# Optimization experiments

Measured on AMD Instinct MI355X. Metric: run time of the kernel, lower is better.

The kernel has to match this reference:

```python
import jax, jax.numpy as jnp
import numpy as np

B, T, F, D, H, L = 4, 1024, 128, 512, 8, 4
DFF = 4 * D
NE, MD = 16, 20
HD = D // H
SCALE = 1.0 / HD ** 0.5


def _ln(x, w, b):
    m = jnp.mean(x, axis=-1, keepdims=True)
    v = jnp.mean((x - m) ** 2, axis=-1, keepdims=True)
    return (x - m) * jax.lax.rsqrt(v + 1e-5) * w + b


def setup_inputs() -> dict:
    key = jax.random.key(0)
    ks = jax.random.split(key, 16)
    rn = lambda k, shape: jax.random.normal(k, shape, jnp.float32) * 0.02
    return {
        'node_features': jax.random.normal(ks[0], (B, T, F), jnp.float32),
        'centrality': jax.random.uniform(ks[1], (B, T), jnp.float32),
        'edge_types': jax.random.randint(ks[2], (B, T, T), 0, NE),
        'sp_dist': jax.random.randint(ks[3], (B, T, T), 0, MD + 1),
        'node_W': rn(ks[4], (F, D)), 'node_b': jnp.zeros((D,), jnp.float32),
        'cent_W': rn(ks[5], (D,)), 'cent_b': jnp.zeros((D,), jnp.float32),
        'edge_emb': rn(ks[6], (NE, H)), 'dist_emb': rn(ks[7], (MD + 1, H)),
        'ln1_w': jnp.ones((L, D), jnp.float32), 'ln1_b': jnp.zeros((L, D), jnp.float32),
        'q_W': rn(ks[8], (L, D, D)), 'q_b': jnp.zeros((L, D), jnp.float32),
        'k_W': rn(ks[9], (L, D, D)), 'k_b': jnp.zeros((L, D), jnp.float32),
        'v_W': rn(ks[10], (L, D, D)), 'v_b': jnp.zeros((L, D), jnp.float32),
        'o_W': rn(ks[11], (L, D, D)), 'o_b': jnp.zeros((L, D), jnp.float32),
        'ln2_w': jnp.ones((L, D), jnp.float32), 'ln2_b': jnp.zeros((L, D), jnp.float32),
        'f1_W': rn(ks[12], (L, D, DFF)), 'f1_b': jnp.zeros((L, DFF), jnp.float32),
        'f2_W': rn(ks[13], (L, DFF, D)), 'f2_b': jnp.zeros((L, D), jnp.float32),
    }


def _forward(node_features, centrality, edge_types, sp_dist,
             node_W, node_b, cent_W, cent_b, edge_emb, dist_emb,
             ln1_w, ln1_b, q_W, q_b, k_W, k_b, v_W, v_b, o_W, o_b,
             ln2_w, ln2_b, f1_W, f1_b, f2_W, f2_b):
    # node embedding + centrality encoding
    h = node_features @ node_W + node_b                      # [B,T,D]
    h = h + centrality[..., None] * cent_W + cent_b          # Linear(1,D)
    # Graphormer attention bias: [B,T,T,H] -> [B,H,T,T]
    sp = jnp.clip(sp_dist, 0, MD)
    attn_bias = (edge_emb[edge_types] + dist_emb[sp]).transpose(0, 3, 1, 2)

    def step(h, p):
        l1w, l1b, qW, qb, kW, kb, vW, vb, oW, ob, l2w, l2b, w1, b1, w2, b2 = p
        x = _ln(h, l1w, l1b)
        q = (x @ qW + qb).reshape(B, T, H, HD)
        k = (x @ kW + kb).reshape(B, T, H, HD)
        v = (x @ vW + vb).reshape(B, T, H, HD)
        scores = jnp.einsum('bihd,bjhd->bhij', q, k) * SCALE + attn_bias
        attn = jax.nn.softmax(scores, axis=-1)
        o = jnp.einsum('bhij,bjhd->bihd', attn, v).reshape(B, T, D)
        h = h + (o @ oW + ob)                                # dropout in eval mode
        x2 = _ln(h, l2w, l2b)
        h = h + (jax.nn.silu(x2 @ w1 + b1) @ w2 + b2)
        return h, None

    layer_params = (ln1_w, ln1_b, q_W, q_b, k_W, k_b, v_W, v_b, o_W, o_b,
                    ln2_w, ln2_b, f1_W, f1_b, f2_W, f2_b)
    h, _ = jax.lax.scan(step, h, layer_params)
    return h


def reference(node_features, centrality, edge_types, sp_dist,
              node_W, node_b, cent_W, cent_b, edge_emb, dist_emb,
              ln1_w, ln1_b, q_W, q_b, k_W, k_b, v_W, v_b, o_W, o_b,
              ln2_w, ln2_b, f1_W, f1_b, f2_W, f2_b):
    return _forward(node_features, centrality, edge_types, sp_dist,
                    node_W, node_b, cent_W, cent_b, edge_emb, dist_emb,
                    ln1_w, ln1_b, q_W, q_b, k_W, k_b, v_W, v_b, o_W, o_b,
                    ln2_w, ln2_b, f1_W, f1_b, f2_W, f2_b)
```

## Files before the change

kernel.cpp:

```cpp
#include <hip/hip_runtime.h>
#include <cstddef>
#include <cstdint>

#define B_    4
#define T_    1024
#define F_    128
#define D_    512
#define H_    8
#define L_    4
#define DFF_  2048
#define HD_   64
#define SCALE_ 0.125f
#define LOG2E_ 1.4426950408889634f
#define CL2E_  (SCALE_ * LOG2E_)

typedef __attribute__((ext_vector_type(8))) short bf16x8;
typedef __attribute__((ext_vector_type(4))) float f32x4;

#define AS1(p) ((const __attribute__((address_space(1))) void*)(p))
#define AS3(p) ((__attribute__((address_space(3))) void*)(p))

__device__ __forceinline__ short f2bf(float f) {
    unsigned u = __float_as_uint(f);
    u += 0x7FFFu + ((u >> 16) & 1u);
    return (short)(u >> 16);
}
__device__ __forceinline__ float bf2f(short s) {
    return __uint_as_float(((unsigned)(unsigned short)s) << 16);
}

__global__ __launch_bounds__(256) void ln_k(
    const float* __restrict__ X, const float* __restrict__ w,
    const float* __restrict__ b, short* __restrict__ Y)
{
    const int row = blockIdx.x;
    const int tid = threadIdx.x;
    const float* xr = X + (size_t)row * D_;
    const float v0 = xr[tid];
    const float v1 = xr[tid + 256];
    float s  = v0 + v1;
    float s2 = v0 * v0 + v1 * v1;
#pragma unroll
    for (int off = 1; off < 64; off <<= 1) {
        s  += __shfl_xor(s,  off);
        s2 += __shfl_xor(s2, off);
    }
    __shared__ float ss[4], ss2[4];
    if ((tid & 63) == 0) { ss[tid >> 6] = s; ss2[tid >> 6] = s2; }
    __syncthreads();
    s  = ss[0]  + ss[1]  + ss[2]  + ss[3];
    s2 = ss2[0] + ss2[1] + ss2[2] + ss2[3];
    const float mean = s * (1.f / D_);
    const float var  = s2 * (1.f / D_) - mean * mean;
    const float r    = rsqrtf(var + 1e-5f);
    short* yr = Y + (size_t)row * D_;
    yr[tid]       = f2bf((v0 - mean) * r * w[tid]       + b[tid]);
    yr[tid + 256] = f2bf((v1 - mean) * r * w[tid + 256] + b[tid + 256]);
}

__global__ __launch_bounds__(256) void transpose_all_k(
    const float* __restrict__ qW, const float* __restrict__ kW,
    const float* __restrict__ vW, const float* __restrict__ oW,
    const float* __restrict__ f1W, const float* __restrict__ f2W,
    const float* __restrict__ nW,
    short* __restrict__ WqkvT, short* __restrict__ WoT,
    short* __restrict__ Wf1T, short* __restrict__ Wf2T,
    short* __restrict__ nWt)
{
    const int id = blockIdx.y;
    const float* src; short* dst; int K, N;
    if (id < 12) {
        const int l = id / 3, which = id % 3;
        const float* s3 = (which == 0) ? qW : (which == 1) ? kW : vW;
        src = s3 + (size_t)l * D_ * D_;
        dst = WqkvT + ((size_t)l * 3 + which) * D_ * D_;
        K = D_; N = D_;
    } else if (id < 16) {
        const int l = id - 12;
        src = oW + (size_t)l * D_ * D_;  dst = WoT + (size_t)l * D_ * D_;
        K = D_; N = D_;
    } else if (id < 20) {
        const int l = id - 16;
        src = f1W + (size_t)l * D_ * DFF_;  dst = Wf1T + (size_t)l * DFF_ * D_;
        K = D_; N = DFF_;
    } else if (id < 24) {
        const int l = id - 20;
        src = f2W + (size_t)l * DFF_ * D_;  dst = Wf2T + (size_t)l * D_ * DFF_;
        K = DFF_; N = D_;
    } else {
        src = nW; dst = nWt; K = F_; N = D_;
    }
    const int ntiles = (K >> 5) * (N >> 5);
    if ((int)blockIdx.x >= ntiles) return;
    const int nt = N >> 5;
    const int k0 = (blockIdx.x / nt) << 5, n0 = (blockIdx.x % nt) << 5;

    __shared__ float t[32][33];
    const int c = threadIdx.x, r0 = threadIdx.y;
#pragma unroll
    for (int i = 0; i < 32; i += 8)
        t[r0 + i][c] = src[(size_t)(k0 + r0 + i) * N + n0 + c];
    __syncthreads();
#pragma unroll
    for (int i = 0; i < 32; i += 8)
        dst[(size_t)(n0 + r0 + i) * K + k0 + c] = f2bf(t[c][r0 + i]);
}

__global__ __launch_bounds__(256) void prep_k(
    const int* __restrict__ et, const int* __restrict__ sp,
    const float* __restrict__ ee, const float* __restrict__ de,
    unsigned char* __restrict__ biasT8,
    const float* __restrict__ nf, short* __restrict__ nfb,
    const float* __restrict__ qb, const float* __restrict__ kb,
    const float* __restrict__ vb, float* __restrict__ biasf)
{
    const int bid = blockIdx.x;
    const int tid = threadIdx.x;
    if (bid >= 4096) {
        if (bid < 4608) {
            const int i = (((bid - 4096) << 8) + tid) << 2;
            const float4 v = *(const float4*)(nf + i);
            *(short4*)(nfb + i) =
                make_short4(f2bf(v.x), f2bf(v.y), f2bf(v.z), f2bf(v.w));
        } else {
            const int i = ((bid - 4608) << 8) + tid;
            const int l = i / 1536, c = i % 1536;
            float v;
            if (c < 512)       v = qb[l * 512 + c];
            else if (c < 1024) v = kb[l * 512 + c - 512];
            else               v = vb[l * 512 + c - 1024];
            biasf[i] = v;
        }
        return;
    }
    __shared__ float eeS[16][8], deS[21][8];
    if (tid < 128) eeS[tid >> 3][tid & 7] = ee[tid];
    for (int t = tid; t < 168; t += 256)
        deS[t >> 3][t & 7] = de[t];
    __syncthreads();
    const int gid = bid * 256 + tid;
    const int j4  = (gid & 255) << 2;
    const int bi  = gid >> 8;
    const size_t base = (size_t)bi * T_ + j4;
    const int4 e = *(const int4*)(et + base);
    const int4 s = *(const int4*)(sp + base);
    const int b = bi >> 10, i = bi & 1023;
    const int ex[4] = {e.x, e.y, e.z, e.w};
    const int sx[4] = {min(s.x, 20), min(s.y, 20), min(s.z, 20), min(s.w, 20)};
#pragma unroll
    for (int h = 0; h < 8; ++h) {
        uchar4 o;
        float v;
        v = (eeS[ex[0]][h] + deS[sx[0]][h]) * LOG2E_ + 0.5f;
        o.x = (unsigned char)(int)fminf(fmaxf(v * 255.f + 0.5f, 0.f), 255.f);
        v = (eeS[ex[1]][h] + deS[sx[1]][h]) * LOG2E_ + 0.5f;
        o.y = (unsigned char)(int)fminf(fmaxf(v * 255.f + 0.5f, 0.f), 255.f);
        v = (eeS[ex[2]][h] + deS[sx[2]][h]) * LOG2E_ + 0.5f;
        o.z = (unsigned char)(int)fminf(fmaxf(v * 255.f + 0.5f, 0.f), 255.f);
        v = (eeS[ex[3]][h] + deS[sx[3]][h]) * LOG2E_ + 0.5f;
        o.w = (unsigned char)(int)fminf(fmaxf(v * 255.f + 0.5f, 0.f), 255.f);
        *(uchar4*)(biasT8 + ((size_t)((b * H_ + h) * T_ + i)) * T_ + j4) = o;
    }
}

__global__ __launch_bounds__(256) void embed_mm_k(
    const short* __restrict__ A, const short* __restrict__ Wt,
    const float* __restrict__ nb, const float* __restrict__ cb,
    const float* __restrict__ cW, const float* __restrict__ cent,
    float* __restrict__ C)
{
    const int K = F_, N = D_;
    __shared__ short As[128 * 32];
    __shared__ short Bs[64 * 32];
    const int tid  = threadIdx.x;
    const int lane = tid & 63, wv = tid >> 6;
    const int bm = blockIdx.y << 7, bn = blockIdx.x << 6;
    const int wm = (wv & 1) << 6, wn = (wv >> 1) << 5;

    const int c0 = (wv << 6) + lane;
    const int m0 = c0 >> 2, q0 = (c0 & 3) ^ ((m0 >> 1) & 3);
    const int c1 = 256 + c0;
    const int m1 = c1 >> 2, q1 = (c1 & 3) ^ ((m1 >> 1) & 3);

    const short* gA0 = A  + (size_t)(bm + m0) * K + (q0 << 3);
    const short* gA1 = A  + (size_t)(bm + m1) * K + (q1 << 3);
    const short* gB0 = Wt + (size_t)(bn + m0) * K + (q0 << 3);

    f32x4 acc[4][2];
#pragma unroll
    for (int i = 0; i < 4; ++i)
#pragma unroll
        for (int j = 0; j < 2; ++j)
            acc[i][j] = (f32x4){0.f, 0.f, 0.f, 0.f};

    const int fm = lane & 15, fq = lane >> 4;
    int caddr[4], baddr[2];
#pragma unroll
    for (int t = 0; t < 4; ++t) {
        const int rowA = wm + (t << 4) + fm;
        caddr[t] = ((rowA << 2) + (fq ^ ((rowA >> 1) & 3))) << 3;
    }
#pragma unroll
    for (int t = 0; t < 2; ++t) {
        const int rowB = wn + (t << 4) + fm;
        baddr[t] = ((rowB << 2) + (fq ^ ((rowB >> 1) & 3))) << 3;
    }

    for (int k0 = 0; k0 < K; k0 += 32) {
        __builtin_amdgcn_global_load_lds(AS1(gA0), AS3(As + (wv << 9)),        16, 0, 0);
        __builtin_amdgcn_global_load_lds(AS1(gA1), AS3(As + 2048 + (wv << 9)), 16, 0, 0);
        __builtin_amdgcn_global_load_lds(AS1(gB0), AS3(Bs + (wv << 9)),        16, 0, 0);
        gA0 += 32; gA1 += 32; gB0 += 32;
        __syncthreads();

        bf16x8 af[4], bf[2];
#pragma unroll
        for (int t = 0; t < 4; ++t) af[t] = *(const bf16x8*)(As + caddr[t]);
#pragma unroll
        for (int t = 0; t < 2; ++t) bf[t] = *(const bf16x8*)(Bs + baddr[t]);
#pragma unroll
        for (int i = 0; i < 4; ++i)
#pragma unroll
            for (int j = 0; j < 2; ++j)
                acc[i][j] = __builtin_amdgcn_mfma_f32_16x16x32_bf16(
                    af[i], bf[j], acc[i][j], 0, 0, 0);
        __syncthreads();
    }

    const int col0 = bn + wn + fm;
    const int row0 = bm + wm + (fq << 2);
#pragma unroll
    for (int j = 0; j < 2; ++j) {
        const int colg = col0 + (j << 4);
        const float bb = nb[colg] + cb[colg];
        const float cw = cW[colg];
#pragma unroll
        for (int i = 0; i < 4; ++i) {
#pragma unroll
            for (int r = 0; r < 4; ++r) {
                const int rowg = row0 + (i << 4) + r;
                C[(size_t)rowg * N + colg] = acc[i][j][r] + bb + cent[rowg] * cw;
            }
        }
    }
}

template <int OUTM, int ACT, int RES>
__global__ __launch_bounds__(256) void mm_k(
    const short* __restrict__ A, const short* __restrict__ Wt,
    const float* __restrict__ bias, const float* __restrict__ R,
    void* __restrict__ Cv, int M, int N, int K)
{
    __shared__ short As[128 * 32];
    __shared__ short Bs[128 * 32];
    const int tid  = threadIdx.x;
    const int lane = tid & 63, wv = tid >> 6;
    const int bm = blockIdx.y << 7, bn = blockIdx.x << 7;
    const int wm = (wv & 1) << 6, wn = (wv >> 1) << 6;

    const int c0 = (wv << 6) + lane;
    const int m0 = c0 >> 2, q0 = (c0 & 3) ^ ((m0 >> 1) & 3);
    const int c1 = 256 + c0;
    const int m1 = c1 >> 2, q1 = (c1 & 3) ^ ((m1 >> 1) & 3);

    const short* gA0 = A  + (size_t)(bm + m0) * K + (q0 << 3);
    const short* gA1 = A  + (size_t)(bm + m1) * K + (q1 << 3);
    const short* gB0 = Wt + (size_t)(bn + m0) * K + (q0 << 3);
    const short* gB1 = Wt + (size_t)(bn + m1) * K + (q1 << 3);

    f32x4 acc[4][4];
#pragma unroll
    for (int i = 0; i < 4; ++i)
#pragma unroll
        for (int j = 0; j < 4; ++j)
            acc[i][j] = (f32x4){0.f, 0.f, 0.f, 0.f};

    const int fm = lane & 15, fq = lane >> 4;
    int caddr[4], baddr[4];
#pragma unroll
    for (int t = 0; t < 4; ++t) {
        const int rowA = wm + (t << 4) + fm;
        caddr[t] = ((rowA << 2) + (fq ^ ((rowA >> 1) & 3))) << 3;
        const int rowB = wn + (t << 4) + fm;
        baddr[t] = ((rowB << 2) + (fq ^ ((rowB >> 1) & 3))) << 3;
    }

    for (int k0 = 0; k0 < K; k0 += 32) {
        __builtin_amdgcn_global_load_lds(AS1(gA0), AS3(As + (wv << 9)),        16, 0, 0);
        __builtin_amdgcn_global_load_lds(AS1(gA1), AS3(As + 2048 + (wv << 9)), 16, 0, 0);
        __builtin_amdgcn_global_load_lds(AS1(gB0), AS3(Bs + (wv << 9)),        16, 0, 0);
        __builtin_amdgcn_global_load_lds(AS1(gB1), AS3(Bs + 2048 + (wv << 9)), 16, 0, 0);
        gA0 += 32; gA1 += 32; gB0 += 32; gB1 += 32;
        __syncthreads();

        bf16x8 af[4], bf[4];
#pragma unroll
        for (int t = 0; t < 4; ++t) {
            af[t] = *(const bf16x8*)(As + caddr[t]);
            bf[t] = *(const bf16x8*)(Bs + baddr[t]);
        }
#pragma unroll
        for (int i = 0; i < 4; ++i)
#pragma unroll
            for (int j = 0; j < 4; ++j)
                acc[i][j] = __builtin_amdgcn_mfma_f32_16x16x32_bf16(
                    af[i], bf[j], acc[i][j], 0, 0, 0);
        __syncthreads();
    }

    const int col0 = bn + wn + fm;
    const int row0 = bm + wm + (fq << 2);
    float* Cf = (float*)Cv;
    short* Cb = (short*)Cv;
#pragma unroll
    for (int j = 0; j < 4; ++j) {
        const int colg = col0 + (j << 4);
        const float bb = bias[colg];
#pragma unroll
        for (int i = 0; i < 4; ++i) {
#pragma unroll
            for (int r = 0; r < 4; ++r) {
                const int rowg = row0 + (i << 4) + r;
                float v = acc[i][j][r] + bb;
                if (ACT) v = v / (1.f + __expf(-v));
                const size_t off = (size_t)rowg * N + colg;
                if (RES) v += R[off];
                if (OUTM == 1) Cb[off] = f2bf(v);
                else           Cf[off] = v;
            }
        }
    }
}

__global__ __launch_bounds__(256) void qkv64_k(
    const short* __restrict__ A, const short* __restrict__ Wt,
    const float* __restrict__ bias, short* __restrict__ QKb,
    short* __restrict__ VtOut)
{
    const int K = D_;
    __shared__ short As[128 * 32];
    __shared__ short Bs[64 * 32];
    const int tid  = threadIdx.x;
    const int lane = tid & 63, wv = tid >> 6;
    const int bm = blockIdx.y << 7, bn = blockIdx.x << 6;
    const int wm = (wv & 1) << 6, wn = (wv >> 1) << 5;

    const int c0 = (wv << 6) + lane;
    const int m0 = c0 >> 2, q0 = (c0 & 3) ^ ((m0 >> 1) & 3);
    const int c1 = 256 + c0;
    const int m1 = c1 >> 2, q1 = (c1 & 3) ^ ((m1 >> 1) & 3);

    const short* gA0 = A  + (size_t)(bm + m0) * K + (q0 << 3);
    const short* gA1 = A  + (size_t)(bm + m1) * K + (q1 << 3);
    const short* gB0 = Wt + (size_t)(bn + m0) * K + (q0 << 3);

    f32x4 acc[4][2];
#pragma unroll
    for (int i = 0; i < 4; ++i)
#pragma unroll
        for (int j = 0; j < 2; ++j)
            acc[i][j] = (f32x4){0.f, 0.f, 0.f, 0.f};

    const int fm = lane & 15, fq = lane >> 4;
    int caddr[4], baddr[2];
#pragma unroll
    for (int t = 0; t < 4; ++t) {
        const int rowA = wm + (t << 4) + fm;
        caddr[t] = ((rowA << 2) + (fq ^ ((rowA >> 1) & 3))) << 3;
    }
#pragma unroll
    for (int t = 0; t < 2; ++t) {
        const int rowB = wn + (t << 4) + fm;
        baddr[t] = ((rowB << 2) + (fq ^ ((rowB >> 1) & 3))) << 3;
    }

    for (int k0 = 0; k0 < K; k0 += 32) {
        __builtin_amdgcn_global_load_lds(AS1(gA0), AS3(As + (wv << 9)),        16, 0, 0);
        __builtin_amdgcn_global_load_lds(AS1(gA1), AS3(As + 2048 + (wv << 9)), 16, 0, 0);
        __builtin_amdgcn_global_load_lds(AS1(gB0), AS3(Bs + (wv << 9)),        16, 0, 0);
        gA0 += 32; gA1 += 32; gB0 += 32;
        __syncthreads();

        bf16x8 af[4], bf[2];
#pragma unroll
        for (int t = 0; t < 4; ++t) af[t] = *(const bf16x8*)(As + caddr[t]);
#pragma unroll
        for (int t = 0; t < 2; ++t) bf[t] = *(const bf16x8*)(Bs + baddr[t]);
#pragma unroll
        for (int i = 0; i < 4; ++i)
#pragma unroll
            for (int j = 0; j < 2; ++j)
                acc[i][j] = __builtin_amdgcn_mfma_f32_16x16x32_bf16(
                    af[i], bf[j], acc[i][j], 0, 0, 0);
        __syncthreads();
    }

    const int col0 = bn + wn + fm;
    const int row0 = bm + wm + (fq << 2);
#pragma unroll
    for (int j = 0; j < 2; ++j) {
        const int colg = col0 + (j << 4);
        const float bb = bias[colg];
#pragma unroll
        for (int i = 0; i < 4; ++i) {
#pragma unroll
            for (int r = 0; r < 4; ++r) {
                const int rowg = row0 + (i << 4) + r;
                const float v = acc[i][j][r] + bb;
                if (colg < 1024) {
                    QKb[(size_t)rowg * 1024 + colg] = f2bf(v);
                } else {
                    const int da = colg - 1024;
                    const int hh = da >> 6, dd = da & 63;
                    const int bb2 = rowg >> 10, tt = rowg & 1023;
                    VtOut[((size_t)(bb2 * H_ + hh) * 64 + dd) * T_ + tt] = f2bf(v);
                }
            }
        }
    }
}

__global__ __launch_bounds__(256) void flash_k(
    const short* __restrict__ QKb, const short* __restrict__ Vt,
    const unsigned char* __restrict__ biasT8, short* __restrict__ OpartB,
    float* __restrict__ Lpart)
{
    const int tid = threadIdx.x;
    const int bx = blockIdx.x;
    const int it = bx >> 1, split = bx & 1;
    const int i0 = it << 6;
    const int h  = blockIdx.y;
    const int b  = blockIdx.z;
    const int lane = tid & 63, w = tid >> 6;
    const int fm = lane & 15, q = lane >> 4;

    __shared__ short Ks[4096];
    __shared__ short Vs[4096];
    __shared__ unsigned char Bsh8[4096];
    __shared__ short Ps[64][72];

    const short* qp = QKb + (size_t)(b * T_ + i0 + (w << 4) + fm) * 1024 + (h << 6) + (q << 3);
    const bf16x8 aq0 = *(const bf16x8*)(qp);
    const bf16x8 aq1 = *(const bf16x8*)(qp + 32);

    const int s0 = (w << 6) + lane, r0 = s0 >> 3, cc0 = (s0 & 7) ^ (r0 & 7);
    const int s1 = 256 + s0,        r1 = s1 >> 3, cc1 = (s1 & 7) ^ (r1 & 7);
    const short* gK0 = QKb + (size_t)(b * T_ + r0) * 1024 + 512 + (h << 6) + (cc0 << 3);
    const short* gK1 = QKb + (size_t)(b * T_ + r1) * 1024 + 512 + (h << 6) + (cc1 << 3);
    const short* gV0 = Vt + ((size_t)((b * H_ + h) << 6) + r0) * T_ + (cc0 << 3);
    const short* gV1 = Vt + ((size_t)((b * H_ + h) << 6) + r1) * T_ + (cc1 << 3);
    const int br = s0 >> 2, bc = (s0 & 3) ^ (br & 3);
    const unsigned char* gB0 = biasT8 +
        ((size_t)(b * H_ + h) * T_ + i0 + br) * T_ + (bc << 4);

    int fAddr[4][2];
#pragma unroll
    for (int t = 0; t < 4; ++t) {
        const int row = (t << 4) + fm;
#pragma unroll
        for (int ks = 0; ks < 2; ++ks)
            fAddr[t][ks] = (row << 6) + (((q + (ks << 2)) ^ (row & 7)) << 3);
    }

    int bAddr[4][4];
#pragma unroll
    for (int r = 0; r < 4; ++r) {
        const int rowL = (w << 4) + (q << 2) + r;
#pragma unroll
        for (int jt = 0; jt < 4; ++jt)
            bAddr[r][jt] = (rowL << 6) + (((jt ^ (rowL & 3))) << 4) + fm;
    }

    const short oneb = 0x3F80;
    const bf16x8 ones = {oneb, oneb, oneb, oneb, oneb, oneb, oneb, oneb};

    f32x4 accO[4];
#pragma unroll
    for (int dt = 0; dt < 4; ++dt) accO[dt] = (f32x4){0.f, 0.f, 0.f, 0.f};
    f32x4 accL = (f32x4){0.f, 0.f, 0.f, 0.f};

    const int irow = b * T_ + i0 + (w << 4) + (q << 2);
    short* psW = &Ps[(w << 4) + (q << 2)][fm];
    const short* psR = &Ps[(w << 4) + fm][q << 3];

    const int jbeg = split << 9, jend = jbeg + 512;
    for (int j0 = jbeg; j0 < jend; j0 += 64) {
        __syncthreads();
        __builtin_amdgcn_global_load_lds(AS1(gK0 + (size_t)j0 * 1024), AS3(Ks + (s0 << 3)), 16, 0, 0);
        __builtin_amdgcn_global_load_lds(AS1(gK1 + (size_t)j0 * 1024), AS3(Ks + (s1 << 3)), 16, 0, 0);
        __builtin_amdgcn_global_load_lds(AS1(gV0 + j0), AS3(Vs + (s0 << 3)), 16, 0, 0);
        __builtin_amdgcn_global_load_lds(AS1(gV1 + j0), AS3(Vs + (s1 << 3)), 16, 0, 0);
        __builtin_amdgcn_global_load_lds(AS1(gB0 + j0), AS3(Bsh8 + (s0 << 4)), 16, 0, 0);
        __syncthreads();

        f32x4 s[4];
#pragma unroll
        for (int jt = 0; jt < 4; ++jt) s[jt] = (f32x4){0.f, 0.f, 0.f, 0.f};
#pragma unroll
        for (int jt = 0; jt < 4; ++jt) {
            const bf16x8 k0 = *(const bf16x8*)(Ks + fAddr[jt][0]);
            const bf16x8 k1 = *(const bf16x8*)(Ks + fAddr[jt][1]);
            s[jt] = __builtin_amdgcn_mfma_f32_16x16x32_bf16(aq0, k0, s[jt], 0, 0, 0);
            s[jt] = __builtin_amdgcn_mfma_f32_16x16x32_bf16(aq1, k1, s[jt], 0, 0, 0);
        }

#pragma unroll
        for (int r = 0; r < 4; ++r)
#pragma unroll
            for (int jt = 0; jt < 4; ++jt) {
                const float q8 = (float)Bsh8[bAddr[r][jt]];
                const float bb = fmaf(q8, 1.f / 255.f, -0.5f);
                const float p = __builtin_amdgcn_exp2f(fmaf(s[jt][r], CL2E_, bb));
                psW[(size_t)r * 72 + (jt << 4)] = f2bf(p);
            }

#pragma unroll
        for (int ks = 0; ks < 2; ++ks) {
            const bf16x8 ap = *(const bf16x8*)(psR + (ks << 5));
            accL = __builtin_amdgcn_mfma_f32_16x16x32_bf16(ap, ones, accL, 0, 0, 0);
#pragma unroll
            for (int dt = 0; dt < 4; ++dt) {
                const bf16x8 bv = *(const bf16x8*)(Vs + fAddr[dt][ks]);
                accO[dt] = __builtin_amdgcn_mfma_f32_16x16x32_bf16(ap, bv, accO[dt], 0, 0, 0);
            }
        }
    }

    short* obase = OpartB + (size_t)split * B_ * T_ * D_;
#pragma unroll
    for (int r = 0; r < 4; ++r) {
        short* op = obase + (size_t)(irow + r) * D_ + (h << 6) + fm;
#pragma unroll
        for (int dt = 0; dt < 4; ++dt)
            op[dt << 4] = f2bf(accO[dt][r]);
    }
    if (fm == 0) {
#pragma unroll
        for (int r = 0; r < 4; ++r)
            Lpart[(size_t)split * B_ * T_ * H_ + (size_t)(irow + r) * H_ + h] = accL[r];
    }
}

__global__ __launch_bounds__(256) void combine_k(
    const short* __restrict__ OpartB, const float* __restrict__ Lpart,
    short* __restrict__ Ob)
{
    const int gid = blockIdx.x * 256 + threadIdx.x;
    const int d4  = (gid & 127) << 2;
    const int row = gid >> 7;
    const int h   = d4 >> 6;
    const float l = Lpart[(size_t)row * H_ + h] +
                    Lpart[(size_t)B_ * T_ * H_ + (size_t)row * H_ + h];
    const float inv = 1.f / l;
    const size_t o = (size_t)row * D_ + d4;
    const short4 a = *(const short4*)(OpartB + o);
    const short4 c = *(const short4*)(OpartB + (size_t)B_ * T_ * D_ + o);
    short4 r = make_short4(
        f2bf((bf2f(a.x) + bf2f(c.x)) * inv), f2bf((bf2f(a.y) + bf2f(c.y)) * inv),
        f2bf((bf2f(a.z) + bf2f(c.z)) * inv), f2bf((bf2f(a.w) + bf2f(c.w)) * inv));
    *(short4*)(Ob + o) = r;
}

__global__ __launch_bounds__(256) void mm64_k(
    const short* __restrict__ A, const short* __restrict__ Wt,
    const float* __restrict__ bias, const float* __restrict__ R,
    float* __restrict__ C, int M, int N, int K)
{
    __shared__ short As[128 * 32];
    __shared__ short Bs[64 * 32];
    const int tid  = threadIdx.x;
    const int lane = tid & 63, wv = tid >> 6;
    const int bm = blockIdx.y << 7, bn = blockIdx.x << 6;
    const int wm = (wv & 1) << 6, wn = (wv >> 1) << 5;

    const int c0 = (wv << 6) + lane;
    const int m0 = c0 >> 2, q0 = (c0 & 3) ^ ((m0 >> 1) & 3);
    const int c1 = 256 + c0;
    const int m1 = c1 >> 2, q1 = (c1 & 3) ^ ((m1 >> 1) & 3);

    const short* gA0 = A  + (size_t)(bm + m0) * K + (q0 << 3);
    const short* gA1 = A  + (size_t)(bm + m1) * K + (q1 << 3);
    const short* gB0 = Wt + (size_t)(bn + m0) * K + (q0 << 3);

    f32x4 acc[4][2];
#pragma unroll
    for (int i = 0; i < 4; ++i)
#pragma unroll
        for (int j = 0; j < 2; ++j)
            acc[i][j] = (f32x4){0.f, 0.f, 0.f, 0.f};

    const int fm = lane & 15, fq = lane >> 4;
    int caddr[4], baddr[2];
#pragma unroll
    for (int t = 0; t < 4; ++t) {
        const int rowA = wm + (t << 4) + fm;
        caddr[t] = ((rowA << 2) + (fq ^ ((rowA >> 1) & 3))) << 3;
    }
#pragma unroll
    for (int t = 0; t < 2; ++t) {
        const int rowB = wn + (t << 4) + fm;
        baddr[t] = ((rowB << 2) + (fq ^ ((rowB >> 1) & 3))) << 3;
    }

    for (int k0 = 0; k0 < K; k0 += 32) {
        __builtin_amdgcn_global_load_lds(AS1(gA0), AS3(As + (wv << 9)),        16, 0, 0);
        __builtin_amdgcn_global_load_lds(AS1(gA1), AS3(As + 2048 + (wv << 9)), 16, 0, 0);
        __builtin_amdgcn_global_load_lds(AS1(gB0), AS3(Bs + (wv << 9)),        16, 0, 0);
        gA0 += 32; gA1 += 32; gB0 += 32;
        __syncthreads();

        bf16x8 af[4], bf[2];
#pragma unroll
        for (int t = 0; t < 4; ++t) af[t] = *(const bf16x8*)(As + caddr[t]);
#pragma unroll
        for (int t = 0; t < 2; ++t) bf[t] = *(const bf16x8*)(Bs + baddr[t]);
#pragma unroll
        for (int i = 0; i < 4; ++i)
#pragma unroll
            for (int j = 0; j < 2; ++j)
                acc[i][j] = __builtin_amdgcn_mfma_f32_16x16x32_bf16(
                    af[i], bf[j], acc[i][j], 0, 0, 0);
        __syncthreads();
    }

    const int col0 = bn + wn + fm;
    const int row0 = bm + wm + (fq << 2);
#pragma unroll
    for (int j = 0; j < 2; ++j) {
        const int colg = col0 + (j << 4);
        const float bb = bias[colg];
#pragma unroll
        for (int i = 0; i < 4; ++i) {
#pragma unroll
            for (int r = 0; r < 4; ++r) {
                const int rowg = row0 + (i << 4) + r;
                const size_t off = (size_t)rowg * N + colg;
                C[off] = acc[i][j][r] + bb + R[off];
            }
        }
    }
}

extern "C" void kernel_launch(void* const* d_in, const int* in_sizes, int n_in,
                              void* d_out, int out_size, void* d_ws, size_t ws_size,
                              hipStream_t stream)
{
    (void)in_sizes; (void)n_in; (void)out_size; (void)ws_size;

    const float* nf   = (const float*)d_in[0];
    const float* cent = (const float*)d_in[1];
    const int*   et   = (const int*)  d_in[2];
    const int*   sp   = (const int*)  d_in[3];
    const float* nW   = (const float*)d_in[4];
    const float* nb   = (const float*)d_in[5];
    const float* cW   = (const float*)d_in[6];
    const float* cb   = (const float*)d_in[7];
    const float* ee   = (const float*)d_in[8];
    const float* de   = (const float*)d_in[9];
    const float* ln1w = (const float*)d_in[10];
    const float* ln1b = (const float*)d_in[11];
    const float* qW   = (const float*)d_in[12];
    const float* qb   = (const float*)d_in[13];
    const float* kW   = (const float*)d_in[14];
    const float* kb   = (const float*)d_in[15];
    const float* vW   = (const float*)d_in[16];
    const float* vb   = (const float*)d_in[17];
    const float* oW   = (const float*)d_in[18];
    const float* ob   = (const float*)d_in[19];
    const float* ln2w = (const float*)d_in[20];
    const float* ln2b = (const float*)d_in[21];
    const float* f1W  = (const float*)d_in[22];
    const float* f1b  = (const float*)d_in[23];
    const float* f2W  = (const float*)d_in[24];
    const float* f2b  = (const float*)d_in[25];

    const int M = B_ * T_;
    char* p = (char*)d_ws;
    float* Hbuf  = (float*)p;  p += (size_t)M * D_ * 4;
    short* QKb   = (short*)p;  p += (size_t)M * 1024 * 2;
    short* Vt    = (short*)p;  p += (size_t)B_ * H_ * 64 * T_ * 2;
    float* biasf = (float*)p;  p += (size_t)L_ * 3 * D_ * 4;
    short* Xbuf  = (short*)p;  p += (size_t)M * D_ * 2;
    short* Ob    = (short*)p;  p += (size_t)M * D_ * 2;
    short* FF    = (short*)p;  p += (size_t)M * DFF_ * 2;
    unsigned char* biasT8 = (unsigned char*)p; p += (size_t)B_ * H_ * T_ * T_;
    short* WqkvT = (short*)p;  p += (size_t)L_ * 3 * D_ * D_ * 2;
    short* WoT   = (short*)p;  p += (size_t)L_ * D_ * D_ * 2;
    short* Wf1T  = (short*)p;  p += (size_t)L_ * DFF_ * D_ * 2;
    short* Wf2T  = (short*)p;  p += (size_t)L_ * D_ * DFF_ * 2;
    short* nfb   = (short*)p;  p += (size_t)M * F_ * 2;
    short* nWt   = (short*)p;  p += (size_t)D_ * F_ * 2;
    short* OpartB = (short*)p; p += (size_t)2 * M * D_ * 2;
    float* Lpart = (float*)p;  p += (size_t)2 * M * H_ * 4;

    float* out = (float*)d_out;

    transpose_all_k<<<dim3(1024, 25), dim3(32, 8), 0, stream>>>(
        qW, kW, vW, oW, f1W, f2W, nW, WqkvT, WoT, Wf1T, Wf2T, nWt);
    prep_k<<<dim3(4632), dim3(256), 0, stream>>>(
        et, sp, ee, de, biasT8, nf, nfb, qb, kb, vb, biasf);
    embed_mm_k<<<dim3(D_ / 64, M / 128), dim3(256), 0, stream>>>(
        nfb, nWt, nb, cb, cW, cent, Hbuf);

    const dim3 blk(256);
    const dim3 gQKV(3 * D_ / 64, M / 128);
    const dim3 gO64(D_ / 64,     M / 128);
    const dim3 gF1 (DFF_ / 128,  M / 128);
    const dim3 gAttn(2 * T_ / 64, H_, B_);
    const dim3 gCmb(M * D_ / 1024);

    for (int l = 0; l < L_; ++l) {
        const size_t bOff  = (size_t)l * D_;
        const size_t b1Off = (size_t)l * DFF_;

        ln_k<<<dim3(M), blk, 0, stream>>>(Hbuf, ln1w + bOff, ln1b + bOff, Xbuf);

        qkv64_k<<<gQKV, blk, 0, stream>>>(
            Xbuf, WqkvT + (size_t)l * 3 * D_ * D_, biasf + (size_t)l * 3 * D_,
            QKb, Vt);

        flash_k<<<gAttn, blk, 0, stream>>>(QKb, Vt, biasT8, OpartB, Lpart);
        combine_k<<<gCmb, blk, 0, stream>>>(OpartB, Lpart, Ob);

        mm64_k<<<gO64, blk, 0, stream>>>(
            Ob, WoT + (size_t)l * D_ * D_, ob + bOff, Hbuf, Hbuf, M, D_, D_);

        ln_k<<<dim3(M), blk, 0, stream>>>(Hbuf, ln2w + bOff, ln2b + bOff, Xbuf);

        mm_k<1, 1, 0><<<gF1, blk, 0, stream>>>(
            Xbuf, Wf1T + (size_t)l * DFF_ * D_, f1b + b1Off, nullptr, FF, M, DFF_, D_);

        float* cdst = (l == L_ - 1) ? out : Hbuf;
        mm64_k<<<gO64, blk, 0, stream>>>(
            FF, Wf2T + (size_t)l * D_ * DFF_, f2b + bOff, Hbuf, cdst, M, D_, DFF_);
    }
}
```

Before: 669.4 us.

## Double-buffer LDS tiles in GEMM and flash-attention kernels to overlap loads

Every GEMM kernel (embed, generic mm, QKV, mm64) and the flash-attention kernel now keep two LDS buffers. The next K/V/bias or A/B tile is issued with global_load_lds into the spare buffer while the current one feeds the MFMAs. This drops one barrier per iteration and hides global-load latency behind compute. In exchange, LDS use per block doubles, which may lower occupancy, especially for the flash kernel.

After: 684.0 us. +2.2%, slower.

```diff
diff --git a/kernel.cpp b/kernel.cpp
--- a/kernel.cpp
+++ b/kernel.cpp
@@ -170,8 +170,8 @@
     float* __restrict__ C)
 {
     const int K = F_, N = D_;
-    __shared__ short As[128 * 32];
-    __shared__ short Bs[64 * 32];
+    __shared__ short As[2][128 * 32];
+    __shared__ short Bs[2][64 * 32];
     const int tid  = threadIdx.x;
     const int lane = tid & 63, wv = tid >> 6;
     const int bm = blockIdx.y << 7, bn = blockIdx.x << 6;
@@ -206,26 +206,33 @@
         baddr[t] = ((rowB << 2) + (fq ^ ((rowB >> 1) & 3))) << 3;
     }
 
+#define EMB_STAGE(KK, BUF) do { \
+    __builtin_amdgcn_global_load_lds(AS1(gA0 + (KK)), AS3(&As[BUF][(wv << 9)]),        16, 0, 0); \
+    __builtin_amdgcn_global_load_lds(AS1(gA1 + (KK)), AS3(&As[BUF][2048 + (wv << 9)]), 16, 0, 0); \
+    __builtin_amdgcn_global_load_lds(AS1(gB0 + (KK)), AS3(&Bs[BUF][(wv << 9)]),        16, 0, 0); \
+} while (0)
+
+    EMB_STAGE(0, 0);
+    int cur = 0;
     for (int k0 = 0; k0 < K; k0 += 32) {
-        __builtin_amdgcn_global_load_lds(AS1(gA0), AS3(As + (wv << 9)),        16, 0, 0);
-        __builtin_amdgcn_global_load_lds(AS1(gA1), AS3(As + 2048 + (wv << 9)), 16, 0, 0);
-        __builtin_amdgcn_global_load_lds(AS1(gB0), AS3(Bs + (wv << 9)),        16, 0, 0);
-        gA0 += 32; gA1 += 32; gB0 += 32;
         __syncthreads();
-
+        if (k0 + 32 < K) EMB_STAGE(k0 + 32, cur ^ 1);
+        const short* Asc = As[cur];
+        const short* Bsc = Bs[cur];
         bf16x8 af[4], bf[2];
 #pragma unroll
-        for (int t = 0; t < 4; ++t) af[t] = *(const bf16x8*)(As + caddr[t]);
-#pragma unroll
-        for (int t = 0; t < 2; ++t) bf[t] = *(const bf16x8*)(Bs + baddr[t]);
+        for (int t = 0; t < 4; ++t) af[t] = *(const bf16x8*)(Asc + caddr[t]);
+#pragma unroll
+        for (int t = 0; t < 2; ++t) bf[t] = *(const bf16x8*)(Bsc + baddr[t]);
 #pragma unroll
         for (int i = 0; i < 4; ++i)
 #pragma unroll
             for (int j = 0; j < 2; ++j)
                 acc[i][j] = __builtin_amdgcn_mfma_f32_16x16x32_bf16(
                     af[i], bf[j], acc[i][j], 0, 0, 0);
-        __syncthreads();
-    }
+        cur ^= 1;
+    }
+#undef EMB_STAGE
 
     const int col0 = bn + wn + fm;
     const int row0 = bm + wm + (fq << 2);
@@ -251,8 +258,8 @@
     const float* __restrict__ bias, const float* __restrict__ R,
     void* __restrict__ Cv, int M, int N, int K)
 {
-    __shared__ short As[128 * 32];
-    __shared__ short Bs[128 * 32];
+    __shared__ short As[2][128 * 32];
+    __shared__ short Bs[2][128 * 32];
     const int tid  = threadIdx.x;
     const int lane = tid & 63, wv = tid >> 6;
     const int bm = blockIdx.y << 7, bn = blockIdx.x << 7;
@@ -285,19 +292,25 @@
         baddr[t] = ((rowB << 2) + (fq ^ ((rowB >> 1) & 3))) << 3;
     }
 
+#define MM_STAGE(KK, BUF) do { \
+    __builtin_amdgcn_global_load_lds(AS1(gA0 + (KK)), AS3(&As[BUF][(wv << 9)]),        16, 0, 0); \
+    __builtin_amdgcn_global_load_lds(AS1(gA1 + (KK)), AS3(&As[BUF][2048 + (wv << 9)]), 16, 0, 0); \
+    __builtin_amdgcn_global_load_lds(AS1(gB0 + (KK)), AS3(&Bs[BUF][(wv << 9)]),        16, 0, 0); \
+    __builtin_amdgcn_global_load_lds(AS1(gB1 + (KK)), AS3(&Bs[BUF][2048 + (wv << 9)]), 16, 0, 0); \
+} while (0)
+
+    MM_STAGE(0, 0);
+    int cur = 0;
     for (int k0 = 0; k0 < K; k0 += 32) {
-        __builtin_amdgcn_global_load_lds(AS1(gA0), AS3(As + (wv << 9)),        16, 0, 0);
-        __builtin_amdgcn_global_load_lds(AS1(gA1), AS3(As + 2048 + (wv << 9)), 16, 0, 0);
-        __builtin_amdgcn_global_load_lds(AS1(gB0), AS3(Bs + (wv << 9)),        16, 0, 0);
-        __builtin_amdgcn_global_load_lds(AS1(gB1), AS3(Bs + 2048 + (wv << 9)), 16, 0, 0);
-        gA0 += 32; gA1 += 32; gB0 += 32; gB1 += 32;
         __syncthreads();
-
+        if (k0 + 32 < K) MM_STAGE(k0 + 32, cur ^ 1);
+        const short* Asc = As[cur];
+        const short* Bsc = Bs[cur];
         bf16x8 af[4], bf[4];
 #pragma unroll
         for (int t = 0; t < 4; ++t) {
-            af[t] = *(const bf16x8*)(As + caddr[t]);
-            bf[t] = *(const bf16x8*)(Bs + baddr[t]);
+            af[t] = *(const bf16x8*)(Asc + caddr[t]);
+            bf[t] = *(const bf16x8*)(Bsc + baddr[t]);
         }
 #pragma unroll
         for (int i = 0; i < 4; ++i)
@@ -305,8 +318,9 @@
             for (int j = 0; j < 4; ++j)
                 acc[i][j] = __builtin_amdgcn_mfma_f32_16x16x32_bf16(
                     af[i], bf[j], acc[i][j], 0, 0, 0);
-        __syncthreads();
-    }
+        cur ^= 1;
+    }
+#undef MM_STAGE
 
     const int col0 = bn + wn + fm;
     const int row0 = bm + wm + (fq << 2);
@@ -338,8 +352,8 @@
     short* __restrict__ VtOut)
 {
     const int K = D_;
-    __shared__ short As[128 * 32];
-    __shared__ short Bs[64 * 32];
+    __shared__ short As[2][128 * 32];
+    __shared__ short Bs[2][64 * 32];
     const int tid  = threadIdx.x;
     const int lane = tid & 63, wv = tid >> 6;
     const int bm = blockIdx.y << 7, bn = blockIdx.x << 6;
@@ -374,26 +388,33 @@
         baddr[t] = ((rowB << 2) + (fq ^ ((rowB >> 1) & 3))) << 3;
     }
 
+#define QKV_STAGE(KK, BUF) do { \
+    __builtin_amdgcn_global_load_lds(AS1(gA0 + (KK)), AS3(&As[BUF][(wv << 9)]),        16, 0, 0); \
+    __builtin_amdgcn_global_load_lds(AS1(gA1 + (KK)), AS3(&As[BUF][2048 + (wv << 9)]), 16, 0, 0); \
+    __builtin_amdgcn_global_load_lds(AS1(gB0 + (KK)), AS3(&Bs[BUF][(wv << 9)]),        16, 0, 0); \
+} while (0)
+
+    QKV_STAGE(0, 0);
+    int cur = 0;
     for (int k0 = 0; k0 < K; k0 += 32) {
-        __builtin_amdgcn_global_load_lds(AS1(gA0), AS3(As + (wv << 9)),        16, 0, 0);
-        __builtin_amdgcn_global_load_lds(AS1(gA1), AS3(As + 2048 + (wv << 9)), 16, 0, 0);
-        __builtin_amdgcn_global_load_lds(AS1(gB0), AS3(Bs + (wv << 9)),        16, 0, 0);
-        gA0 += 32; gA1 += 32; gB0 += 32;
         __syncthreads();
-
+        if (k0 + 32 < K) QKV_STAGE(k0 + 32, cur ^ 1);
+        const short* Asc = As[cur];
+        const short* Bsc = Bs[cur];
         bf16x8 af[4], bf[2];
 #pragma unroll
-        for (int t = 0; t < 4; ++t) af[t] = *(const bf16x8*)(As + caddr[t]);
-#pragma unroll
-        for (int t = 0; t < 2; ++t) bf[t] = *(const bf16x8*)(Bs + baddr[t]);
+        for (int t = 0; t < 4; ++t) af[t] = *(const bf16x8*)(Asc + caddr[t]);
+#pragma unroll
+        for (int t = 0; t < 2; ++t) bf[t] = *(const bf16x8*)(Bsc + baddr[t]);
 #pragma unroll
         for (int i = 0; i < 4; ++i)
 #pragma unroll
             for (int j = 0; j < 2; ++j)
                 acc[i][j] = __builtin_amdgcn_mfma_f32_16x16x32_bf16(
                     af[i], bf[j], acc[i][j], 0, 0, 0);
-        __syncthreads();
-    }
+        cur ^= 1;
+    }
+#undef QKV_STAGE
 
     const int col0 = bn + wn + fm;
     const int row0 = bm + wm + (fq << 2);
@@ -434,9 +455,9 @@
     const int lane = tid & 63, w = tid >> 6;
     const int fm = lane & 15, q = lane >> 4;
 
-    __shared__ short Ks[4096];
-    __shared__ short Vs[4096];
-    __shared__ unsigned char Bsh8[4096];
+    __shared__ short Ks[2][4096];
+    __shared__ short Vs[2][4096];
+    __shared__ unsigned char Bsh8[2][4096];
     __shared__ short Ps[64][72];
 
     const short* qp = QKb + (size_t)(b * T_ + i0 + (w << 4) + fm) * 1024 + (h << 6) + (q << 3);
@@ -483,23 +504,31 @@
     short* psW = &Ps[(w << 4) + (q << 2)][fm];
     const short* psR = &Ps[(w << 4) + fm][q << 3];
 
+#define FLASH_STAGE(J0, BUF) do { \
+    __builtin_amdgcn_global_load_lds(AS1(gK0 + (size_t)(J0) * 1024), AS3(&Ks[BUF][s0 << 3]), 16, 0, 0); \
+    __builtin_amdgcn_global_load_lds(AS1(gK1 + (size_t)(J0) * 1024), AS3(&Ks[BUF][s1 << 3]), 16, 0, 0); \
+    __builtin_amdgcn_global_load_lds(AS1(gV0 + (J0)), AS3(&Vs[BUF][s0 << 3]), 16, 0, 0); \
+    __builtin_amdgcn_global_load_lds(AS1(gV1 + (J0)), AS3(&Vs[BUF][s1 << 3]), 16, 0, 0); \
+    __builtin_amdgcn_global_load_lds(AS1(gB0 + (J0)), AS3(&Bsh8[BUF][s0 << 4]), 16, 0, 0); \
+} while (0)
+
     const int jbeg = split << 9, jend = jbeg + 512;
+    FLASH_STAGE(jbeg, 0);
+    int cur = 0;
     for (int j0 = jbeg; j0 < jend; j0 += 64) {
         __syncthreads();
-        __builtin_amdgcn_global_load_lds(AS1(gK0 + (size_t)j0 * 1024), AS3(Ks + (s0 << 3)), 16, 0, 0);
-        __builtin_amdgcn_global_load_lds(AS1(gK1 + (size_t)j0 * 1024), AS3(Ks + (s1 << 3)), 16, 0, 0);
-        __builtin_amdgcn_global_load_lds(AS1(gV0 + j0), AS3(Vs + (s0 << 3)), 16, 0, 0);
-        __builtin_amdgcn_global_load_lds(AS1(gV1 + j0), AS3(Vs + (s1 << 3)), 16, 0, 0);
-        __builtin_amdgcn_global_load_lds(AS1(gB0 + j0), AS3(Bsh8 + (s0 << 4)), 16, 0, 0);
-        __syncthreads();
+        if (j0 + 64 < jend) FLASH_STAGE(j0 + 64, cur ^ 1);
+        const short* Ksc = Ks[cur];
+        const short* Vsc = Vs[cur];
+        const unsigned char* Bc = Bsh8[cur];
 
         f32x4 s[4];
 #pragma unroll
         for (int jt = 0; jt < 4; ++jt) s[jt] = (f32x4){0.f, 0.f, 0.f, 0.f};
 #pragma unroll
         for (int jt = 0; jt < 4; ++jt) {
-            const bf16x8 k0 = *(const bf16x8*)(Ks + fAddr[jt][0]);
-            const bf16x8 k1 = *(const bf16x8*)(Ks + fAddr[jt][1]);
+            const bf16x8 k0 = *(const bf16x8*)(Ksc + fAddr[jt][0]);
+            const bf16x8 k1 = *(const bf16x8*)(Ksc + fAddr[jt][1]);
             s[jt] = __builtin_amdgcn_mfma_f32_16x16x32_bf16(aq0, k0, s[jt], 0, 0, 0);
             s[jt] = __builtin_amdgcn_mfma_f32_16x16x32_bf16(aq1, k1, s[jt], 0, 0, 0);
         }
@@ -508,7 +537,7 @@
         for (int r = 0; r < 4; ++r)
 #pragma unroll
             for (int jt = 0; jt < 4; ++jt) {
-                const float q8 = (float)Bsh8[bAddr[r][jt]];
+                const float q8 = (float)Bc[bAddr[r][jt]];
                 const float bb = fmaf(q8, 1.f / 255.f, -0.5f);
                 const float p = __builtin_amdgcn_exp2f(fmaf(s[jt][r], CL2E_, bb));
                 psW[(size_t)r * 72 + (jt << 4)] = f2bf(p);
@@ -520,11 +549,13 @@
             accL = __builtin_amdgcn_mfma_f32_16x16x32_bf16(ap, ones, accL, 0, 0, 0);
 #pragma unroll
             for (int dt = 0; dt < 4; ++dt) {
-                const bf16x8 bv = *(const bf16x8*)(Vs + fAddr[dt][ks]);
+                const bf16x8 bv = *(const bf16x8*)(Vsc + fAddr[dt][ks]);
                 accO[dt] = __builtin_amdgcn_mfma_f32_16x16x32_bf16(ap, bv, accO[dt], 0, 0, 0);
             }
         }
-    }
+        cur ^= 1;
+    }
+#undef FLASH_STAGE
 
     short* obase = OpartB + (size_t)split * B_ * T_ * D_;
 #pragma unroll
@@ -566,8 +597,8 @@
     const float* __restrict__ bias, const float* __restrict__ R,
     float* __restrict__ C, int M, int N, int K)
 {
-    __shared__ short As[128 * 32];
-    __shared__ short Bs[64 * 32];
+    __shared__ short As[2][128 * 32];
+    __shared__ short Bs[2][64 * 32];
     const int tid  = threadIdx.x;
     const int lane = tid & 63, wv = tid >> 6;
     const int bm = blockIdx.y << 7, bn = blockIdx.x << 6;
@@ -602,26 +633,33 @@
         baddr[t] = ((rowB << 2) + (fq ^ ((rowB >> 1) & 3))) << 3;
     }
 
+#define MM64_STAGE(KK, BUF) do { \
+    __builtin_amdgcn_global_load_lds(AS1(gA0 + (KK)), AS3(&As[BUF][(wv << 9)]),        16, 0, 0); \
+    __builtin_amdgcn_global_load_lds(AS1(gA1 + (KK)), AS3(&As[BUF][2048 + (wv << 9)]), 16, 0, 0); \
+    __builtin_amdgcn_global_load_lds(AS1(gB0 + (KK)), AS3(&Bs[BUF][(wv << 9)]),        16, 0, 0); \
+} while (0)
+
+    MM64_STAGE(0, 0);
+    int cur = 0;
     for (int k0 = 0; k0 < K; k0 += 32) {
-        __builtin_amdgcn_global_load_lds(AS1(gA0), AS3(As + (wv << 9)),        16, 0, 0);
-        __builtin_amdgcn_global_load_lds(AS1(gA1), AS3(As + 2048 + (wv << 9)), 16, 0, 0);
-        __builtin_amdgcn_global_load_lds(AS1(gB0), AS3(Bs + (wv << 9)),        16, 0, 0);
-        gA0 += 32; gA1 += 32; gB0 += 32;
         __syncthreads();
-
+        if (k0 + 32 < K) MM64_STAGE(k0 + 32, cur ^ 1);
+        const short* Asc = As[cur];
+        const short* Bsc = Bs[cur];
         bf16x8 af[4], bf[2];
 #pragma unroll
-        for (int t = 0; t < 4; ++t) af[t] = *(const bf16x8*)(As + caddr[t]);
-#pragma unroll
-        for (int t = 0; t < 2; ++t) bf[t] = *(const bf16x8*)(Bs + baddr[t]);
+        for (int t = 0; t < 4; ++t) af[t] = *(const bf16x8*)(Asc + caddr[t]);
+#pragma unroll
+        for (int t = 0; t < 2; ++t) bf[t] = *(const bf16x8*)(Bsc + baddr[t]);
 #pragma unroll
         for (int i = 0; i < 4; ++i)
 #pragma unroll
             for (int j = 0; j < 2; ++j)
                 acc[i][j] = __builtin_amdgcn_mfma_f32_16x16x32_bf16(
                     af[i], bf[j], acc[i][j], 0, 0, 0);
-        __syncthreads();
-    }
+        cur ^= 1;
+    }
+#undef MM64_STAGE
 
     const int col0 = bn + wn + fm;
     const int row0 = bm + wm + (fq << 2);
```

## Add 4-stage LDS prefetch pipeline and XCD-aware block remap to GEMM kernels

Applied to the files above, without the earlier changes.

Turns the single-buffered global-to-LDS loop in all four GEMM kernels into a 4-buffer pipeline that keeps three stages in flight. Each iteration waits with partial vmcnt counts and one barrier instead of two __syncthreads, so global loads overlap MFMA work. It also replaces the 2D grid with a 1D grid remapped so consecutive blocks on each XCD share the same row band, aiming for better L2 reuse. The cost is four times the LDS per block, which may reduce occupancy, and the hand-tuned vmcnt values must stay correct.

New measurement: 655.8 us. -2.0%, faster.

```diff
diff --git a/kernel.cpp b/kernel.cpp
--- a/kernel.cpp
+++ b/kernel.cpp
@@ -28,6 +28,13 @@
 __device__ __forceinline__ float bf2f(short s) {
     return __uint_as_float(((unsigned)(unsigned short)s) << 16);
 }
+
+#define PIPE_BARRIER(rem, W2, W1)                                             \
+    if ((rem) >= 2)      asm volatile("s_waitcnt vmcnt(" #W2 ")" ::: "memory"); \
+    else if ((rem) == 1) asm volatile("s_waitcnt vmcnt(" #W1 ")" ::: "memory"); \
+    else                 asm volatile("s_waitcnt vmcnt(0)"      ::: "memory"); \
+    __builtin_amdgcn_s_barrier();                                             \
+    __builtin_amdgcn_sched_barrier(0);
 
 __global__ __launch_bounds__(256) void ln_k(
     const float* __restrict__ X, const float* __restrict__ w,
@@ -170,11 +177,14 @@
     float* __restrict__ C)
 {
     const int K = F_, N = D_;
-    __shared__ short As[128 * 32];
-    __shared__ short Bs[64 * 32];
+    __shared__ short As[4][128 * 32];
+    __shared__ short Bs[4][64 * 32];
     const int tid  = threadIdx.x;
     const int lane = tid & 63, wv = tid >> 6;
-    const int bm = blockIdx.y << 7, bn = blockIdx.x << 6;
+    const int lb = blockIdx.x;
+    const int xcd = lb & 7, jj = lb >> 3;
+    const int bx = jj & 7, by = (xcd << 2) + (jj >> 3);
+    const int bm = by << 7, bn = bx << 6;
     const int wm = (wv & 1) << 6, wn = (wv >> 1) << 5;
 
     const int c0 = (wv << 6) + lane;
@@ -206,26 +216,33 @@
         baddr[t] = ((rowB << 2) + (fq ^ ((rowB >> 1) & 3))) << 3;
     }
 
-    for (int k0 = 0; k0 < K; k0 += 32) {
-        __builtin_amdgcn_global_load_lds(AS1(gA0), AS3(As + (wv << 9)),        16, 0, 0);
-        __builtin_amdgcn_global_load_lds(AS1(gA1), AS3(As + 2048 + (wv << 9)), 16, 0, 0);
-        __builtin_amdgcn_global_load_lds(AS1(gB0), AS3(Bs + (wv << 9)),        16, 0, 0);
-        gA0 += 32; gA1 += 32; gB0 += 32;
-        __syncthreads();
-
+#define EMB_STAGE(KK, BUF) do { \
+    __builtin_amdgcn_global_load_lds(AS1(gA0 + (KK)), AS3(&As[BUF][(wv << 9)]),        16, 0, 0); \
+    __builtin_amdgcn_global_load_lds(AS1(gA1 + (KK)), AS3(&As[BUF][2048 + (wv << 9)]), 16, 0, 0); \
+    __builtin_amdgcn_global_load_lds(AS1(gB0 + (KK)), AS3(&Bs[BUF][(wv << 9)]),        16, 0, 0); \
+} while (0)
+
+    EMB_STAGE(0, 0); EMB_STAGE(32, 1); EMB_STAGE(64, 2);
+    const int nt = K >> 5;
+    for (int t = 0; t < nt; ++t) {
+        const int rem = nt - 1 - t;
+        PIPE_BARRIER(rem, 6, 3);
+        if (rem >= 3) EMB_STAGE((t + 3) << 5, (t + 3) & 3);
+        const short* Asc = As[t & 3];
+        const short* Bsc = Bs[t & 3];
         bf16x8 af[4], bf[2];
 #pragma unroll
-        for (int t = 0; t < 4; ++t) af[t] = *(const bf16x8*)(As + caddr[t]);
-#pragma unroll
-        for (int t = 0; t < 2; ++t) bf[t] = *(const bf16x8*)(Bs + baddr[t]);
+        for (int u = 0; u < 4; ++u) af[u] = *(const bf16x8*)(Asc + caddr[u]);
+#pragma unroll
+        for (int u = 0; u < 2; ++u) bf[u] = *(const bf16x8*)(Bsc + baddr[u]);
 #pragma unroll
         for (int i = 0; i < 4; ++i)
 #pragma unroll
             for (int j = 0; j < 2; ++j)
                 acc[i][j] = __builtin_amdgcn_mfma_f32_16x16x32_bf16(
                     af[i], bf[j], acc[i][j], 0, 0, 0);
-        __syncthreads();
-    }
+    }
+#undef EMB_STAGE
 
     const int col0 = bn + wn + fm;
     const int row0 = bm + wm + (fq << 2);
@@ -251,11 +268,14 @@
     const float* __restrict__ bias, const float* __restrict__ R,
     void* __restrict__ Cv, int M, int N, int K)
 {
-    __shared__ short As[128 * 32];
-    __shared__ short Bs[128 * 32];
+    __shared__ short As[4][128 * 32];
+    __shared__ short Bs[4][128 * 32];
     const int tid  = threadIdx.x;
     const int lane = tid & 63, wv = tid >> 6;
-    const int bm = blockIdx.y << 7, bn = blockIdx.x << 7;
+    const int lb = blockIdx.x;
+    const int xcd = lb & 7, jj = lb >> 3;
+    const int bx = jj & 15, by = (xcd << 2) + (jj >> 4);
+    const int bm = by << 7, bn = bx << 7;
     const int wm = (wv & 1) << 6, wn = (wv >> 1) << 6;
 
     const int c0 = (wv << 6) + lane;
@@ -285,19 +305,26 @@
         baddr[t] = ((rowB << 2) + (fq ^ ((rowB >> 1) & 3))) << 3;
     }
 
-    for (int k0 = 0; k0 < K; k0 += 32) {
-        __builtin_amdgcn_global_load_lds(AS1(gA0), AS3(As + (wv << 9)),        16, 0, 0);
-        __builtin_amdgcn_global_load_lds(AS1(gA1), AS3(As + 2048 + (wv << 9)), 16, 0, 0);
-        __builtin_amdgcn_global_load_lds(AS1(gB0), AS3(Bs + (wv << 9)),        16, 0, 0);
-        __builtin_amdgcn_global_load_lds(AS1(gB1), AS3(Bs + 2048 + (wv << 9)), 16, 0, 0);
-        gA0 += 32; gA1 += 32; gB0 += 32; gB1 += 32;
-        __syncthreads();
-
+#define MM_STAGE(KK, BUF) do { \
+    __builtin_amdgcn_global_load_lds(AS1(gA0 + (KK)), AS3(&As[BUF][(wv << 9)]),        16, 0, 0); \
+    __builtin_amdgcn_global_load_lds(AS1(gA1 + (KK)), AS3(&As[BUF][2048 + (wv << 9)]), 16, 0, 0); \
+    __builtin_amdgcn_global_load_lds(AS1(gB0 + (KK)), AS3(&Bs[BUF][(wv << 9)]),        16, 0, 0); \
+    __builtin_amdgcn_global_load_lds(AS1(gB1 + (KK)), AS3(&Bs[BUF][2048 + (wv << 9)]), 16, 0, 0); \
+} while (0)
+
+    MM_STAGE(0, 0); MM_STAGE(32, 1); MM_STAGE(64, 2);
+    const int nt = K >> 5;
+    for (int t = 0; t < nt; ++t) {
+        const int rem = nt - 1 - t;
+        PIPE_BARRIER(rem, 8, 4);
+        if (rem >= 3) MM_STAGE((t + 3) << 5, (t + 3) & 3);
+        const short* Asc = As[t & 3];
+        const short* Bsc = Bs[t & 3];
         bf16x8 af[4], bf[4];
 #pragma unroll
-        for (int t = 0; t < 4; ++t) {
-            af[t] = *(const bf16x8*)(As + caddr[t]);
-            bf[t] = *(const bf16x8*)(Bs + baddr[t]);
+        for (int u = 0; u < 4; ++u) {
+            af[u] = *(const bf16x8*)(Asc + caddr[u]);
+            bf[u] = *(const bf16x8*)(Bsc + baddr[u]);
         }
 #pragma unroll
         for (int i = 0; i < 4; ++i)
@@ -305,8 +332,8 @@
             for (int j = 0; j < 4; ++j)
                 acc[i][j] = __builtin_amdgcn_mfma_f32_16x16x32_bf16(
                     af[i], bf[j], acc[i][j], 0, 0, 0);
-        __syncthreads();
-    }
+    }
+#undef MM_STAGE
 
     const int col0 = bn + wn + fm;
     const int row0 = bm + wm + (fq << 2);
@@ -338,11 +365,15 @@
     short* __restrict__ VtOut)
 {
     const int K = D_;
-    __shared__ short As[128 * 32];
-    __shared__ short Bs[64 * 32];
+    __shared__ short As[4][128 * 32];
+    __shared__ short Bs[4][64 * 32];
     const int tid  = threadIdx.x;
     const int lane = tid & 63, wv = tid >> 6;
-    const int bm = blockIdx.y << 7, bn = blockIdx.x << 6;
+    const int lb = blockIdx.x;
+    const int xcd = lb & 7, jj = lb >> 3;
+    const int yl = jj / 24, bx = jj - yl * 24;
+    const int by = (xcd << 2) + yl;
+    const int bm = by << 7, bn = bx << 6;
     const int wm = (wv & 1) << 6, wn = (wv >> 1) << 5;
 
     const int c0 = (wv << 6) + lane;
@@ -374,26 +405,33 @@
         baddr[t] = ((rowB << 2) + (fq ^ ((rowB >> 1) & 3))) << 3;
     }
 
-    for (int k0 = 0; k0 < K; k0 += 32) {
-        __builtin_amdgcn_global_load_lds(AS1(gA0), AS3(As + (wv << 9)),        16, 0, 0);
-        __builtin_amdgcn_global_load_lds(AS1(gA1), AS3(As + 2048 + (wv << 9)), 16, 0, 0);
-        __builtin_amdgcn_global_load_lds(AS1(gB0), AS3(Bs + (wv << 9)),        16, 0, 0);
-        gA0 += 32; gA1 += 32; gB0 += 32;
-        __syncthreads();
-
+#define QKV_STAGE(KK, BUF) do { \
+    __builtin_amdgcn_global_load_lds(AS1(gA0 + (KK)), AS3(&As[BUF][(wv << 9)]),        16, 0, 0); \
+    __builtin_amdgcn_global_load_lds(AS1(gA1 + (KK)), AS3(&As[BUF][2048 + (wv << 9)]), 16, 0, 0); \
+    __builtin_amdgcn_global_load_lds(AS1(gB0 + (KK)), AS3(&Bs[BUF][(wv << 9)]),        16, 0, 0); \
+} while (0)
+
+    QKV_STAGE(0, 0); QKV_STAGE(32, 1); QKV_STAGE(64, 2);
+    const int nt = K >> 5;
+    for (int t = 0; t < nt; ++t) {
+        const int rem = nt - 1 - t;
+        PIPE_BARRIER(rem, 6, 3);
+        if (rem >= 3) QKV_STAGE((t + 3) << 5, (t + 3) & 3);
+        const short* Asc = As[t & 3];
+        const short* Bsc = Bs[t & 3];
         bf16x8 af[4], bf[2];
 #pragma unroll
-        for (int t = 0; t < 4; ++t) af[t] = *(const bf16x8*)(As + caddr[t]);
-#pragma unroll
-        for (int t = 0; t < 2; ++t) bf[t] = *(const bf16x8*)(Bs + baddr[t]);
+        for (int u = 0; u < 4; ++u) af[u] = *(const bf16x8*)(Asc + caddr[u]);
+#pragma unroll
+        for (int u = 0; u < 2; ++u) bf[u] = *(const bf16x8*)(Bsc + baddr[u]);
 #pragma unroll
         for (int i = 0; i < 4; ++i)
 #pragma unroll
             for (int j = 0; j < 2; ++j)
                 acc[i][j] = __builtin_amdgcn_mfma_f32_16x16x32_bf16(
                     af[i], bf[j], acc[i][j], 0, 0, 0);
-        __syncthreads();
-    }
+    }
+#undef QKV_STAGE
 
     const int col0 = bn + wn + fm;
     const int row0 = bm + wm + (fq << 2);
@@ -566,11 +604,14 @@
     const float* __restrict__ bias, const float* __restrict__ R,
     float* __restrict__ C, int M, int N, int K)
 {
-    __shared__ short As[128 * 32];
-    __shared__ short Bs[64 * 32];
+    __shared__ short As[4][128 * 32];
+    __shared__ short Bs[4][64 * 32];
     const int tid  = threadIdx.x;
     const int lane = tid & 63, wv = tid >> 6;
-    const int bm = blockIdx.y << 7, bn = blockIdx.x << 6;
+    const int lb = blockIdx.x;
+    const int xcd = lb & 7, jj = lb >> 3;
+    const int bx = jj & 7, by = (xcd << 2) + (jj >> 3);
+    const int bm = by << 7, bn = bx << 6;
     const int wm = (wv & 1) << 6, wn = (wv >> 1) << 5;
 
     const int c0 = (wv << 6) + lane;
@@ -602,26 +643,33 @@
         baddr[t] = ((rowB << 2) + (fq ^ ((rowB >> 1) & 3))) << 3;
     }
 
-    for (int k0 = 0; k0 < K; k0 += 32) {
-        __builtin_amdgcn_global_load_lds(AS1(gA0), AS3(As + (wv << 9)),        16, 0, 0);
-        __builtin_amdgcn_global_load_lds(AS1(gA1), AS3(As + 2048 + (wv << 9)), 16, 0, 0);
-        __builtin_amdgcn_global_load_lds(AS1(gB0), AS3(Bs + (wv << 9)),        16, 0, 0);
-        gA0 += 32; gA1 += 32; gB0 += 32;
-        __syncthreads();
-
+#define MM64_STAGE(KK, BUF) do { \
+    __builtin_amdgcn_global_load_lds(AS1(gA0 + (KK)), AS3(&As[BUF][(wv << 9)]),        16, 0, 0); \
+    __builtin_amdgcn_global_load_lds(AS1(gA1 + (KK)), AS3(&As[BUF][2048 + (wv << 9)]), 16, 0, 0); \
+    __builtin_amdgcn_global_load_lds(AS1(gB0 + (KK)), AS3(&Bs[BUF][(wv << 9)]),        16, 0, 0); \
+} while (0)
+
+    MM64_STAGE(0, 0); MM64_STAGE(32, 1); MM64_STAGE(64, 2);
+    const int nt = K >> 5;
+    for (int t = 0; t < nt; ++t) {
+        const int rem = nt - 1 - t;
+        PIPE_BARRIER(rem, 6, 3);
+        if (rem >= 3) MM64_STAGE((t + 3) << 5, (t + 3) & 3);
+        const short* Asc = As[t & 3];
+        const short* Bsc = Bs[t & 3];
         bf16x8 af[4], bf[2];
 #pragma unroll
-        for (int t = 0; t < 4; ++t) af[t] = *(const bf16x8*)(As + caddr[t]);
-#pragma unroll
-        for (int t = 0; t < 2; ++t) bf[t] = *(const bf16x8*)(Bs + baddr[t]);
+        for (int u = 0; u < 4; ++u) af[u] = *(const bf16x8*)(Asc + caddr[u]);
+#pragma unroll
+        for (int u = 0; u < 2; ++u) bf[u] = *(const bf16x8*)(Bsc + baddr[u]);
 #pragma unroll
         for (int i = 0; i < 4; ++i)
 #pragma unroll
             for (int j = 0; j < 2; ++j)
                 acc[i][j] = __builtin_amdgcn_mfma_f32_16x16x32_bf16(
                     af[i], bf[j], acc[i][j], 0, 0, 0);
-        __syncthreads();
-    }
+    }
+#undef MM64_STAGE
 
     const int col0 = bn + wn + fm;
     const int row0 = bm + wm + (fq << 2);
@@ -699,13 +747,13 @@
         qW, kW, vW, oW, f1W, f2W, nW, WqkvT, WoT, Wf1T, Wf2T, nWt);
     prep_k<<<dim3(4632), dim3(256), 0, stream>>>(
         et, sp, ee, de, biasT8, nf, nfb, qb, kb, vb, biasf);
-    embed_mm_k<<<dim3(D_ / 64, M / 128), dim3(256), 0, stream>>>(
+    embed_mm_k<<<dim3(256), dim3(256), 0, stream>>>(
         nfb, nWt, nb, cb, cW, cent, Hbuf);
 
     const dim3 blk(256);
-    const dim3 gQKV(3 * D_ / 64, M / 128);
-    const dim3 gO64(D_ / 64,     M / 128);
-    const dim3 gF1 (DFF_ / 128,  M / 128);
+    const dim3 gQKV(768);
+    const dim3 gO64(256);
+    const dim3 gF1 (512);
     const dim3 gAttn(2 * T_ / 64, H_, B_);
     const dim3 gCmb(M * D_ / 1024);
 
```
